# Optimization experiments

Measured on AMD Instinct MI355X. Metric: run time of the kernel, lower is better.

Reference implementation:

```python
import jax, jax.numpy as jnp
import numpy as np
from functools import partial

EDGES = [(1,2),(1,3),(1,4),(1,5),(1,6),(2,3),(2,7),(2,8),(3,4),(3,9),(4,5),(4,10),(5,6),(5,11),(6,12),(6,13),(7,8),(7,14),(8,9),(8,14),(9,10),(9,15),(10,11),(10,16),(11,12),(11,17),(12,13),(12,18),(13,18),(14,15),(14,19),(15,16),(15,19),(16,17),(16,20),(17,18),(17,21),(18,21),(19,20),(19,22),(20,21),(20,22),(21,22),(24,25),(24,29),(25,26),(25,29),(26,17),(26,30),(27,28),(27,31),(28,31),(29,30),(29,32),(30,31),(30,32),(31,32),(34,35),(34,39),(35,36),(35,39),(36,37),(36,30),(37,18),(37,41),(38,41),(39,40),(39,42),(30,41),(30,42),(31,42),(44,45),(44,49),(45,46),(45,49),(46,47),(46,50),(47,48),(47,51),(48,51),(49,50),(49,52),(50,51),(50,52),(51,52),(54,55),(54,59),(55,56),(55,59),(56,57),(56,60),(57,58),(57,61),(58,61),(59,60),(59,62),(50,61),(60,62),(61,62)]

B, C, T = 32, 64, 4000
F1, D, F2, NCLS = 8, 2, 16, 4
KLEN, GK = 64, 8


def _bn_pack(k, c):
    kg, kb = jax.random.split(k)
    g = jax.random.uniform(kg, (c,), minval=0.5, maxval=1.5)
    b = 0.1 * jax.random.normal(kb, (c,))
    return jnp.stack([g, b, jnp.zeros(c), jnp.ones(c)])  # gamma, beta, mean, var


def setup_inputs() -> dict:
    key = jax.random.key(0)
    ks = jax.random.split(key, 16)
    A = np.zeros((C, C), np.float32)
    for i, j in EDGES:
        A[i - 1, j - 1] = 1.0
        A[j - 1, i - 1] = 1.0
    np.fill_diagonal(A, 1.0)
    feat = F2 * ((T // 4 + 1) // 8)  # 16 * 125 = 2000
    s = 0.1
    return {
        "x": jax.random.normal(ks[0], (B, C, T), jnp.float32),
        "adjacency": jnp.asarray(A),
        "conv1_w": s * jax.random.normal(ks[1], (F1, 1, 1, KLEN), jnp.float32),
        "bnF1": jnp.stack([_bn_pack(jax.random.fold_in(ks[2], i), F1) for i in range(4)]),
        "imp": jax.random.normal(ks[3], (3, F1, C, C), jnp.float32),
        "gconv_w": s * jax.random.normal(ks[4], (3, F1, F1, 1, GK), jnp.float32),
        "dw_w": s * jax.random.normal(ks[5], (F1 * D, 1, C, 1), jnp.float32),
        "bn_sp": _bn_pack(ks[6], F1 * D),
        "sep_dw_w": s * jax.random.normal(ks[7], (F1 * D, 1, 1, 16), jnp.float32),
        "sep_pw_w": s * jax.random.normal(ks[8], (F2, F1 * D, 1, 1), jnp.float32),
        "bn_sep": _bn_pack(ks[9], F2),
        "fc_w": s * jax.random.normal(ks[10], (NCLS, feat), jnp.float32),
        "fc_b": jnp.zeros((NCLS,), jnp.float32),
    }


def _conv(x, w, pad, groups=1):
    return jax.lax.conv_general_dilated(
        x, w, (1, 1), pad, dimension_numbers=("NCHW", "OIHW", "NCHW"),
        feature_group_count=groups)


def _bn(x, p, eps=1e-3):
    g, b, m, v = p
    scale = g * jax.lax.rsqrt(v + eps)
    return x * scale[None, :, None, None] + (b - m * scale)[None, :, None, None]


def reference(x, adjacency, conv1_w, bnF1, imp, gconv_w, dw_w, bn_sp,
              sep_dw_w, sep_pw_w, bn_sep, fc_w, fc_b):
    Bv = x.shape[0]
    h = x[:, None, :, :]                                    # (B,1,C,T)
    h = _conv(h, conv1_w, [(0, 0), (31, 32)])                # 'same' for k=64
    h = _bn(h, bnF1[0])
    for l in range(3):                                       # GraphTemporalConvolution x3
        A = adjacency[None] * imp[l]                         # (F1,C,C) masked importance
        h = jnp.einsum("fcd,bfdt->bfct", A, h)
        h = _conv(h, gconv_w[l], [(0, 0), (3, 4)])           # 'same' for k=8
        h = jax.nn.elu(_bn(h, bnF1[l + 1]))
    # spatial depthwise conv with max-norm constraint (renorm, no grad through scale)
    norms = jnp.sqrt(jnp.sum(dw_w ** 2, axis=(1, 2, 3), keepdims=True))
    scale = jax.lax.stop_gradient(jnp.minimum(1.0, 1.0 / jnp.maximum(norms, 1e-7)))
    h = _conv(h, dw_w * scale, [(0, 0), (0, 0)], groups=F1)  # (B,F1*D,1,T)
    h = jax.nn.elu(_bn(h, bn_sp))
    h = h.reshape(Bv, F1 * D, 1, T // 4, 4).mean(-1)         # AvgPool (1,4)
    # separable conv
    h = _conv(h, sep_dw_w, [(0, 0), (8, 8)], groups=F1 * D)  # width T/4 + 1
    h = _conv(h, sep_pw_w, [(0, 0), (0, 0)])
    h = jax.nn.elu(_bn(h, bn_sep))
    W = h.shape[-1]
    Wp = (W // 8) * 8
    h = h[..., :Wp].reshape(Bv, F2, 1, Wp // 8, 8).mean(-1)  # AvgPool (1,8)
    feat = h.reshape(Bv, -1)
    return feat @ fc_w.T + fc_b
```

## Files before the change

### kernel.cpp

```cpp
#include <hip/hip_runtime.h>


#define B_   32
#define C_   64
#define T_   4000
#define F1_  8
#define TP_  1000
#define W2_  1001
#define MAXDEG 16
#define ROW4 130
#define ROWD 520

typedef _Float16 h16x2 __attribute__((ext_vector_type(2)));
typedef _Float16 f16x8 __attribute__((ext_vector_type(8)));
typedef float    f32x4 __attribute__((ext_vector_type(4)));
typedef __fp16   cvt16x2 __attribute__((ext_vector_type(2)));

static __device__ __forceinline__ float bf2f(unsigned short h) {
  union { unsigned int u; float f; } v; v.u = ((unsigned int)h) << 16; return v.f;
}
static __device__ __forceinline__ unsigned short f2bf(float f) {
  union { float f; unsigned int u; } v; v.f = f;
  unsigned int r = v.u + 0x7FFFu + ((v.u >> 16) & 1u);
  return (unsigned short)(r >> 16);
}
static __device__ __forceinline__ float lo_h(unsigned int u) {
  union { unsigned int u; _Float16 h[2]; } v; v.u = u; return (float)v.h[0];
}
static __device__ __forceinline__ unsigned int pack2h(float a, float b) {
  union { _Float16 h[2]; unsigned int u; } v;
  v.h[0] = (_Float16)a; v.h[1] = (_Float16)b; return v.u;
}
#if defined(__has_builtin) && __has_builtin(__builtin_amdgcn_cvt_pkrtz)
static __device__ __forceinline__ unsigned int pkh(float a, float b) {
  union { cvt16x2 h; unsigned int u; } v;
  v.h = __builtin_amdgcn_cvt_pkrtz(a, b);
  return v.u;
}
#else
static __device__ __forceinline__ unsigned int pkh(float a, float b) {
  return pack2h(a, b);
}
#endif
static __device__ __forceinline__ h16x2 as_h2(unsigned int u) {
  union { unsigned int u; h16x2 h; } v; v.u = u; return v.h;
}
static __device__ __forceinline__ unsigned int alignb(unsigned int hi,
                                                      unsigned int lo,
                                                      unsigned int s) {
  return (unsigned int)(((((unsigned long long)hi) << 32) | lo) >> s);
}
static __device__ __forceinline__ float swz8(float v) {
  union { float f; int i; } a; a.f = v;
  a.i = __builtin_amdgcn_ds_swizzle(a.i, 0x201F);
  return a.f;
}
#define PERM_LO(y, x) __builtin_amdgcn_perm((y), (x), 0x05040100u)
#define PERM_HI(y, x) __builtin_amdgcn_perm((y), (x), 0x07060302u)
#if defined(__has_builtin) && __has_builtin(__builtin_amdgcn_fdot2)
#define DOT2(a, b, c) __builtin_amdgcn_fdot2((a), (b), (c), false)
#else
static __device__ __forceinline__ float dot2_fb(h16x2 a, h16x2 b, float c) {
  return fmaf((float)a[0], (float)b[0], fmaf((float)a[1], (float)b[1], c));
}
#define DOT2(a, b, c) dot2_fb((a), (b), (c))
#endif
static __device__ __forceinline__ float eluf(float z) {
  return z > 0.0f ? z : __expf(z) - 1.0f;
}
static __device__ __forceinline__ float ldin(const void* p, int i, int isf32) {
  return isf32 ? ((const float*)p)[i] : bf2f(((const unsigned short*)p)[i]);
}

__global__ __launch_bounds__(256) void k0_setup(
    const void* __restrict__ adj, const void* __restrict__ imp,
    const void* __restrict__ dww, const void* __restrict__ w1,
    const void* __restrict__ bnF, const void* __restrict__ gw,
    const void* __restrict__ bnsp, const void* __restrict__ sdw,
    const void* __restrict__ pw, const void* __restrict__ bnsep,
    const void* __restrict__ fcw, const void* __restrict__ fcb,
    int* __restrict__ flag, int* __restrict__ deg, int* __restrict__ col,
    uint4* __restrict__ w1mf,
    uint4* __restrict__ wmf, float* __restrict__ dwn,
    float* __restrict__ sdwc, float* __restrict__ pwc,
    float* __restrict__ fcwc, float* __restrict__ fcbc,
    float* __restrict__ bnFs, float* __restrict__ bnsps,
    float* __restrict__ bnseps,
    unsigned int* __restrict__ dwph)
{
  __shared__ float dwr[1024];
  __shared__ float dsc[16];
  int tid = threadIdx.x;
  int isf32 = (((const float*)adj)[0] == 1.0f) ? 1 : 0;
  if (tid == 0) *flag = isf32;

  for (int idx = tid; idx < 128; idx += 256) {
    int kk = idx >> 6, l = idx & 63;
    int o = l & 15, q = l >> 4;
    uint4 v; v.x = 0u; v.y = 0u; v.z = 0u; v.w = 0u;
    if (o < 8) {
      int bi = o*64 + 32*kk + 8*q;
      v.x = pack2h(ldin(w1, bi+0, isf32), ldin(w1, bi+1, isf32));
      v.y = pack2h(ldin(w1, bi+2, isf32), ldin(w1, bi+3, isf32));
      v.z = pack2h(ldin(w1, bi+4, isf32), ldin(w1, bi+5, isf32));
      v.w = pack2h(ldin(w1, bi+6, isf32), ldin(w1, bi+7, isf32));
    }
    w1mf[idx] = v;
  }
  for (int idx = tid; idx < 384; idx += 256) {
    int lf = idx >> 6;
    int layer = lf >> 1, frag = lf & 1;
    int lane2 = idx & 63;
    int o = lane2 & 15, ii = (lane2 >> 4) + 4*frag;
    uint4 v; v.x = 0u; v.y = 0u; v.z = 0u; v.w = 0u;
    if (o < 8) {
      int bi = layer*512 + (o*8 + ii)*8;
      v.x = pack2h(ldin(gw, bi+0, isf32), ldin(gw, bi+1, isf32));
      v.y = pack2h(ldin(gw, bi+2, isf32), ldin(gw, bi+3, isf32));
      v.z = pack2h(ldin(gw, bi+4, isf32), ldin(gw, bi+5, isf32));
      v.w = pack2h(ldin(gw, bi+6, isf32), ldin(gw, bi+7, isf32));
    }
    wmf[idx] = v;
  }
  for (int i = tid; i < 256;  i += 256) sdwc[i] = ldin(sdw, i, isf32);
  for (int i = tid; i < 256;  i += 256) pwc[i]  = ldin(pw, i, isf32);
  for (int i = tid; i < 8000; i += 256) fcwc[i] = ldin(fcw, i, isf32);
  if (tid < 4) fcbc[tid] = ldin(fcb, tid, isf32);
  for (int i = tid; i < 1024; i += 256) dwr[i] = ldin(dww, i, isf32);

  if (tid < 64) {
    int c = tid, n = 0;
    for (int e = 0; e < MAXDEG; ++e) col[c*MAXDEG + e] = c;
    for (int d = 0; d < 64; ++d) {
      if (ldin(adj, c*64 + d, isf32) != 0.0f) {
        if (n < MAXDEG) col[c*MAXDEG + n] = d;
        ++n;
      }
    }
    deg[c] = n < MAXDEG ? n : MAXDEG;
  }
  __syncthreads();
  if (tid < 16) {
    float s2 = 0.0f;
    for (int c2 = 0; c2 < 64; ++c2) { float wv = dwr[tid*64 + c2]; s2 += wv*wv; }
    dsc[tid] = fminf(1.0f, 1.0f / fmaxf(sqrtf(s2), 1e-7f));
  }
  if (tid >= 64 && tid < 96) {
    int i = tid - 64, s = i >> 3, f = i & 7;
    float g = ldin(bnF, s*32 + f,      isf32);
    float b = ldin(bnF, s*32 + 8 + f,  isf32);
    float m = ldin(bnF, s*32 + 16 + f, isf32);
    float v = ldin(bnF, s*32 + 24 + f, isf32);
    float sc = g * rsqrtf(v + 1e-3f);
    bnFs[s*16 + f] = sc; bnFs[s*16 + 8 + f] = b - m*sc;
  }
  if (tid >= 96 && tid < 112) {
    int ch = tid - 96;
    float g = ldin(bnsp, ch, isf32), b = ldin(bnsp, 16 + ch, isf32);
    float m = ldin(bnsp, 32 + ch, isf32), v = ldin(bnsp, 48 + ch, isf32);
    float sc = g * rsqrtf(v + 1e-3f);
    bnsps[ch] = sc; bnsps[16 + ch] = b - m*sc;
  }
  if (tid >= 112 && tid < 128) {
    int ch = tid - 112;
    float g = ldin(bnsep, ch, isf32), b = ldin(bnsep, 16 + ch, isf32);
    float m = ldin(bnsep, 32 + ch, isf32), v = ldin(bnsep, 48 + ch, isf32);
    float sc = g * rsqrtf(v + 1e-3f);
    bnseps[ch] = sc; bnseps[16 + ch] = b - m*sc;
  }
  __syncthreads();
  for (int i = tid; i < 1024; i += 256) dwn[i] = dwr[i] * dsc[i >> 6];
  __syncthreads();
  for (int idx = tid; idx < 512; idx += 256) {
    int ch = idx >> 5, p = idx & 31;
    dwph[idx] = pack2h(dwr[ch*64 + 2*p]   * dsc[ch],
                       dwr[ch*64 + 2*p+1] * dsc[ch]);
  }
}

__global__ __launch_bounds__(256) void k0b_avals(
    const void* __restrict__ adj, const void* __restrict__ imp,
    const int* __restrict__ flag,
    const int* __restrict__ deg, const int* __restrict__ col,
    float* __restrict__ avals, unsigned int* __restrict__ avph)
{
  int combo = blockIdx.x * 256 + threadIdx.x;
  int isf32 = *flag;
  int c = combo & 63;
  int lf = combo >> 6;
  int dg = deg[c];
  float av[MAXDEG];
  for (int e = 0; e < MAXDEG; ++e) {
    float v = 0.0f;
    if (e < dg) {
      int d = col[c*MAXDEG + e];
      v = ldin(adj, c*64 + d, isf32) * ldin(imp, (lf*64 + c)*64 + d, isf32);
    }
    av[e] = v;
    avals[combo*MAXDEG + e] = v;
  }
  for (int p = 0; p < 8; ++p)
    avph[combo*8 + p] = pack2h(av[2*p], av[2*p + 1]);
}

__global__ __launch_bounds__(256, 4) void k1_conv1_bn(
    const void* __restrict__ x,
    const uint4* __restrict__ w1mf,
    const float* __restrict__ bnFs,
    const int* __restrict__ flag,
    unsigned short* __restrict__ outp)
{
  __shared__ __align__(16) unsigned int xs[548];
  int tid = threadIdx.x;
  int bc = blockIdx.y;
  int b = bc >> 6, c = bc & 63;
  int tb = blockIdx.x * 1024;
  int isf32 = *flag;
  int row = bc * T_;
  if (isf32) {
    const float* xr = (const float*)x + row;
    for (int m = tid; m < 274; m += 256) {
      int tg = tb - 36 + 4*m;
      uint2 st;
      if (tg >= 0 && tg + 3 < T_) {
        float4 v = *(const float4*)(xr + tg);
        st.x = pkh(v.x, v.y); st.y = pkh(v.z, v.w);
      } else {
        float q0 = (tg   >= 0 && tg   < T_) ? xr[tg]   : 0.0f;
        float q1 = (tg+1 >= 0 && tg+1 < T_) ? xr[tg+1] : 0.0f;
        float q2 = (tg+2 >= 0 && tg+2 < T_) ? xr[tg+2] : 0.0f;
        float q3 = (tg+3 >= 0 && tg+3 < T_) ? xr[tg+3] : 0.0f;
        st.x = pkh(q0, q1); st.y = pkh(q2, q3);
      }
      *(uint2*)(xs + 2*m) = st;
    }
  } else {
    const unsigned short* xr = (const unsigned short*)x + row;
    for (int m = tid; m < 274; m += 256) {
      int tg = tb - 36 + 4*m;
      uint2 st;
      if (tg >= 0 && tg + 3 < T_) {
        uint2 v = *(const uint2*)(xr + tg);
        st.x = pkh(bf2f((unsigned short)(v.x & 0xFFFFu)),
                   bf2f((unsigned short)(v.x >> 16)));
        st.y = pkh(bf2f((unsigned short)(v.y & 0xFFFFu)),
                   bf2f((unsigned short)(v.y >> 16)));
      } else {
        float q0 = (tg   >= 0 && tg   < T_) ? bf2f(xr[tg])   : 0.0f;
        float q1 = (tg+1 >= 0 && tg+1 < T_) ? bf2f(xr[tg+1]) : 0.0f;
        float q2 = (tg+2 >= 0 && tg+2 < T_) ? bf2f(xr[tg+2]) : 0.0f;
        float q3 = (tg+3 >= 0 && tg+3 < T_) ? bf2f(xr[tg+3]) : 0.0f;
        st.x = pkh(q0, q1); st.y = pkh(q2, q3);
      }
      *(uint2*)(xs + 2*m) = st;
    }
  }
  __syncthreads();

  int lane = tid & 63;
  int wv4 = tid >> 6;
  int m = lane & 15, q = lane >> 4;
  int sel = (m >> 3) & 1;
  union { uint4 u; f16x8 h; } w0u, w1u;
  w0u.u = w1mf[lane];
  w1u.u = w1mf[64 + lane];
  int o8 = m & 7;
  float sc  = bnFs[o8];
  float shb = bnFs[8 + o8];
  const unsigned int* p0 = xs + 2 + m + 4*q + 128*wv4;
  unsigned short* orow = outp + (size_t)((b*8 + o8)*64 + c) * T_;
  #pragma unroll
  for (int s = 0; s < 8; ++s) {
    unsigned dwa[5], dwb[5];
    #pragma unroll
    for (int j = 0; j < 5; ++j) {
      dwa[j] = p0[16*s + j];
      dwb[j] = p0[16*s + 16 + j];
    }
    union { unsigned d[4]; f16x8 h; } Ae0, Ao0, Ae1, Ao1;
    #pragma unroll
    for (int j = 0; j < 4; ++j) {
      Ao0.d[j] = dwa[j+1];
      Ae0.d[j] = alignb(dwa[j+1], dwa[j], 16);
      Ao1.d[j] = dwb[j+1];
      Ae1.d[j] = alignb(dwb[j+1], dwb[j], 16);
    }
    f32x4 ae = {0.0f, 0.0f, 0.0f, 0.0f};
    f32x4 ao = {0.0f, 0.0f, 0.0f, 0.0f};
    ae = __builtin_amdgcn_mfma_f32_16x16x32_f16(Ae0.h, w0u.h, ae, 0, 0, 0);
    ae = __builtin_amdgcn_mfma_f32_16x16x32_f16(Ae1.h, w1u.h, ae, 0, 0, 0);
    ao = __builtin_amdgcn_mfma_f32_16x16x32_f16(Ao0.h, w0u.h, ao, 0, 0, 0);
    ao = __builtin_amdgcn_mfma_f32_16x16x32_f16(Ao1.h, w1u.h, ao, 0, 0, 0);
    float r0 = swz8(ae[2]);
    float r1 = swz8(ao[2]);
    float r2 = swz8(ae[3]);
    float r3 = swz8(ao[3]);
    float y0 = sel ? r0 : ae[0];
    float y1 = sel ? r1 : ao[0];
    float y2 = sel ? r2 : ae[1];
    float y3 = sel ? r3 : ao[1];
    int t0g = tb + wv4*256 + s*32 + 8*q + 4*sel;
    if (t0g < T_) {
      uint2 st;
      st.x = pkh(y0*sc + shb, y1*sc + shb);
      st.y = pkh(y2*sc + shb, y3*sc + shb);
      *(uint2*)(orow + t0g) = st;
    }
  }
}

__global__ __launch_bounds__(256, 6) void k23_gcn_gconv(
    const unsigned short* __restrict__ in,
    unsigned short* __restrict__ outp,
    const int* __restrict__ deg, const int* __restrict__ col,
    const float* __restrict__ avals,
    const unsigned int* __restrict__ avph,
    const uint4* __restrict__ wmf,
    const float* __restrict__ bnFs, int l)
{
  __shared__ __align__(16) uint4 ash[8 * ROW4];
  int tid = threadIdx.x;
  int wgid = blockIdx.y * 4 + blockIdx.x;
  int swz  = (wgid & 7) * 1024 + (wgid >> 3);
  int c = swz & 63;
  int xt = (swz >> 6) & 3;
  int b = swz >> 8;
  int tb = xt * 1024;
  int wb = tb - 8;
  int dg = deg[c];
  const int* cp = col + c*MAXDEG;

  {
    int i = tid >> 5;
    int mlane = tid & 31;
    int dgp = (dg + 1) >> 1;
    const unsigned int* wpp = avph + ((l*8 + i)*64 + c) * 8;
    const float* av = avals + ((l*8 + i)*64 + c) * MAXDEG;
    const unsigned short* rbp = in + (size_t)((b*8 + i) * 64) * T_;
    for (int m = mlane; m < ROW4; m += 32) {
      int t = wb + 8*m;
      float a[8] = {0,0,0,0,0,0,0,0};
      if (t >= 0 && t + 7 < T_) {
        for (int p = 0; p < dgp; ++p) {
          int d0 = cp[2*p];
          int d1 = cp[2*p + 1];
          h16x2 w2 = as_h2(wpp[p]);
          uint4 v0 = *(const uint4*)(rbp + d0*T_ + t);
          uint4 v1 = *(const uint4*)(rbp + d1*T_ + t);
          a[0] = DOT2(as_h2(PERM_LO(v1.x, v0.x)), w2, a[0]);
          a[1] = DOT2(as_h2(PERM_HI(v1.x, v0.x)), w2, a[1]);
          a[2] = DOT2(as_h2(PERM_LO(v1.y, v0.y)), w2, a[2]);
          a[3] = DOT2(as_h2(PERM_HI(v1.y, v0.y)), w2, a[3]);
          a[4] = DOT2(as_h2(PERM_LO(v1.z, v0.z)), w2, a[4]);
          a[5] = DOT2(as_h2(PERM_HI(v1.z, v0.z)), w2, a[5]);
          a[6] = DOT2(as_h2(PERM_LO(v1.w, v0.w)), w2, a[6]);
          a[7] = DOT2(as_h2(PERM_HI(v1.w, v0.w)), w2, a[7]);
        }
      } else if (t + 7 >= 0 && t < T_) {
        for (int e = 0; e < dg; ++e) {
          int d = cp[e];
          float wv = av[e];
          const unsigned short* rp = rbp + d*T_;
          #pragma unroll
          for (int q = 0; q < 8; ++q) {
            int tq = t + q;
            if (tq >= 0 && tq < T_)
              a[q] = fmaf(wv, lo_h((unsigned int)rp[tq]), a[q]);
          }
        }
      }
      uint4 o;
      o.x = pkh(a[0], a[1]); o.y = pkh(a[2], a[3]);
      o.z = pkh(a[4], a[5]); o.w = pkh(a[6], a[7]);
      ash[i*ROW4 + m] = o;
    }
  }
  __syncthreads();

  int lane = tid & 63;
  int wv4 = tid >> 6;
  int m = lane & 15, q = lane >> 4;
  int sel = (m >> 3) & 1;
  union { uint4 u; f16x8 h; } w0u, w1u;
  w0u.u = wmf[(l*2 + 0)*64 + lane];
  w1u.u = wmf[(l*2 + 1)*64 + lane];
  int o8 = m & 7;
  float sc  = bnFs[(l+1)*16 + o8];
  float shb = bnFs[(l+1)*16 + 8 + o8];
  const unsigned int* ashd = (const unsigned int*)ash;
  const unsigned int* p0 = ashd + q*ROWD + wv4*128 + m + 2;
  const unsigned int* p1 = p0 + 4*ROWD;
  unsigned short* orow = outp + (size_t)((b*8 + o8)*64 + c) * T_;
  #pragma unroll
  for (int s = 0; s < 8; ++s) {
    unsigned dwa[5], dwb[5];
    #pragma unroll
    for (int j = 0; j < 5; ++j) {
      dwa[j] = p0[16*s + j];
      dwb[j] = p1[16*s + j];
    }
    union { unsigned d[4]; f16x8 h; } Ae0, Ao0, Ae1, Ao1;
    #pragma unroll
    for (int j = 0; j < 4; ++j) {
      Ao0.d[j] = dwa[j+1];
      Ae0.d[j] = alignb(dwa[j+1], dwa[j], 16);
      Ao1.d[j] = dwb[j+1];
      Ae1.d[j] = alignb(dwb[j+1], dwb[j], 16);
    }
    f32x4 ae = {0.0f, 0.0f, 0.0f, 0.0f};
    f32x4 ao = {0.0f, 0.0f, 0.0f, 0.0f};
    ae = __builtin_amdgcn_mfma_f32_16x16x32_f16(Ae0.h, w0u.h, ae, 0, 0, 0);
    ae = __builtin_amdgcn_mfma_f32_16x16x32_f16(Ae1.h, w1u.h, ae, 0, 0, 0);
    ao = __builtin_amdgcn_mfma_f32_16x16x32_f16(Ao0.h, w0u.h, ao, 0, 0, 0);
    ao = __builtin_amdgcn_mfma_f32_16x16x32_f16(Ao1.h, w1u.h, ao, 0, 0, 0);
    float r0 = swz8(ae[2]);
    float r1 = swz8(ao[2]);
    float r2 = swz8(ae[3]);
    float r3 = swz8(ao[3]);
    float y0 = sel ? r0 : ae[0];
    float y1 = sel ? r1 : ao[0];
    float y2 = sel ? r2 : ae[1];
    float y3 = sel ? r3 : ao[1];
    int t0g = tb + wv4*256 + s*32 + 8*q + 4*sel;
    if (t0g < T_) {
      uint2 st;
      st.x = pkh(eluf(y0*sc + shb), eluf(y1*sc + shb));
      st.y = pkh(eluf(y2*sc + shb), eluf(y3*sc + shb));
      *(uint2*)(orow + t0g) = st;
    }
  }
}

__global__ __launch_bounds__(256) void k4_dw(
    const unsigned short* __restrict__ in,
    const unsigned int* __restrict__ dwph,
    const float* __restrict__ bnsps,
    float* __restrict__ p1)
{
  int tid = threadIdx.x;
  int bg = blockIdx.y;
  int b = bg >> 3, g = bg & 7;
  int tile = blockIdx.x * 256 + tid;
  if (tile >= 500) return;
  int t0 = tile * 8;
  int base = bg * (64 * T_);
  const unsigned int* w0pp = dwph + (2*g)*32;
  const unsigned int* w1pp = dwph + (2*g + 1)*32;
  float a0[8] = {0,0,0,0,0,0,0,0}, a1[8] = {0,0,0,0,0,0,0,0};
  for (int p = 0; p < 32; ++p) {
    h16x2 w02 = as_h2(w0pp[p]);
    h16x2 w12 = as_h2(w1pp[p]);
    uint4 v0 = *(const uint4*)(in + base + (2*p)*T_ + t0);
    uint4 v1 = *(const uint4*)(in + base + (2*p + 1)*T_ + t0);
    unsigned pr;
    pr = PERM_LO(v1.x, v0.x);
    a0[0] = DOT2(as_h2(pr), w02, a0[0]); a1[0] = DOT2(as_h2(pr), w12, a1[0]);
    pr = PERM_HI(v1.x, v0.x);
    a0[1] = DOT2(as_h2(pr), w02, a0[1]); a1[1] = DOT2(as_h2(pr), w12, a1[1]);
    pr = PERM_LO(v1.y, v0.y);
    a0[2] = DOT2(as_h2(pr), w02, a0[2]); a1[2] = DOT2(as_h2(pr), w12, a1[2]);
    pr = PERM_HI(v1.y, v0.y);
    a0[3] = DOT2(as_h2(pr), w02, a0[3]); a1[3] = DOT2(as_h2(pr), w12, a1[3]);
    pr = PERM_LO(v1.z, v0.z);
    a0[4] = DOT2(as_h2(pr), w02, a0[4]); a1[4] = DOT2(as_h2(pr), w12, a1[4]);
    pr = PERM_HI(v1.z, v0.z);
    a0[5] = DOT2(as_h2(pr), w02, a0[5]); a1[5] = DOT2(as_h2(pr), w12, a1[5]);
    pr = PERM_LO(v1.w, v0.w);
    a0[6] = DOT2(as_h2(pr), w02, a0[6]); a1[6] = DOT2(as_h2(pr), w12, a1[6]);
    pr = PERM_HI(v1.w, v0.w);
    a0[7] = DOT2(as_h2(pr), w02, a0[7]); a1[7] = DOT2(as_h2(pr), w12, a1[7]);
  }
  float sc0 = bnsps[2*g],     sh0 = bnsps[16 + 2*g];
  float sc1 = bnsps[2*g + 1], sh1 = bnsps[16 + 2*g + 1];
  int oi = t0 >> 2;
  float2 r0, r1;
  r0.x = 0.25f * (eluf(a0[0]*sc0+sh0) + eluf(a0[1]*sc0+sh0)
                + eluf(a0[2]*sc0+sh0) + eluf(a0[3]*sc0+sh0));
  r0.y = 0.25f * (eluf(a0[4]*sc0+sh0) + eluf(a0[5]*sc0+sh0)
                + eluf(a0[6]*sc0+sh0) + eluf(a0[7]*sc0+sh0));
  r1.x = 0.25f * (eluf(a1[0]*sc1+sh1) + eluf(a1[1]*sc1+sh1)
                + eluf(a1[2]*sc1+sh1) + eluf(a1[3]*sc1+sh1));
  r1.y = 0.25f * (eluf(a1[4]*sc1+sh1) + eluf(a1[5]*sc1+sh1)
                + eluf(a1[6]*sc1+sh1) + eluf(a1[7]*sc1+sh1));
  *(float2*)(p1 + (b*16 + 2*g)*TP_ + oi)     = r0;
  *(float2*)(p1 + (b*16 + 2*g + 1)*TP_ + oi) = r1;
}

__global__ __launch_bounds__(256) void k5_sep(
    const float* __restrict__ p1,
    const float* __restrict__ sdwc,
    const float* __restrict__ pwc,
    const float* __restrict__ bnseps,
    float* __restrict__ p2)
{
  __shared__ float ps[16*272];
  int tid = threadIdx.x;
  int wq = blockIdx.x, b = blockIdx.y;
  int wb = wq * 256;
  for (int ch = 0; ch < 16; ++ch) {
    for (int s = tid; s < 272; s += 256) {
      int t = wb - 8 + s;
      ps[ch*272 + s] = (t >= 0 && t < TP_) ? p1[(b*16 + ch)*TP_ + t] : 0.0f;
    }
  }
  __syncthreads();
  int w0 = wb + tid;
  if (w0 >= W2_) return;
  float dws[16];
  for (int ch = 0; ch < 16; ++ch) {
    float a = 0.0f;
    #pragma unroll
    for (int k = 0; k < 16; ++k)
      a = fmaf(sdwc[ch*16 + k], ps[ch*272 + tid + k], a);
    dws[ch] = a;
  }
  for (int f = 0; f < 16; ++f) {
    float a = 0.0f;
    #pragma unroll
    for (int ch = 0; ch < 16; ++ch) a = fmaf(pwc[f*16 + ch], dws[ch], a);
    float sc = bnseps[f], sh = bnseps[16 + f];
    p2[(b*16 + f)*W2_ + w0] = eluf(a*sc + sh);
  }
}

__global__ __launch_bounds__(256) void k6_fc(
    const float* __restrict__ p2,
    const float* __restrict__ fcwc,
    const float* __restrict__ fcbc,
    const int* __restrict__ flag,
    void* __restrict__ outp)
{
  __shared__ float red[4*256];
  int tid = threadIdx.x;
  int b = blockIdx.x;
  float part[4] = {0.0f, 0.0f, 0.0f, 0.0f};
  for (int idx = tid; idx < 2000; idx += 256) {
    int f = idx / 125, q = idx - f*125;
    const float* src = p2 + (b*16 + f)*W2_ + q*8;
    float s = src[0]+src[1]+src[2]+src[3]+src[4]+src[5]+src[6]+src[7];
    float mval = 0.125f * s;
    #pragma unroll
    for (int n = 0; n < 4; ++n) part[n] = fmaf(fcwc[n*2000 + idx], mval, part[n]);
  }
  #pragma unroll
  for (int n = 0; n < 4; ++n) red[n*256 + tid] = part[n];
  __syncthreads();
  for (int s = 128; s > 0; s >>= 1) {
    if (tid < s) {
      #pragma unroll
      for (int n = 0; n < 4; ++n) red[n*256 + tid] += red[n*256 + tid + s];
    }
    __syncthreads();
  }
  if (tid < 4) {
    float val = red[tid*256] + fcbc[tid];
    if (*flag) ((float*)outp)[b*4 + tid] = val;
    else       ((unsigned short*)outp)[b*4 + tid] = f2bf(val);
  }
}

extern "C" void kernel_launch(void* const* d_in, const int* in_sizes, int n_in,
                              void* d_out, int out_size, void* d_ws, size_t ws_size,
                              hipStream_t stream) {
  const void* x     = d_in[0];
  const void* adj   = d_in[1];
  const void* w1    = d_in[2];
  const void* bnF   = d_in[3];
  const void* imp   = d_in[4];
  const void* gw    = d_in[5];
  const void* dww   = d_in[6];
  const void* bnsp  = d_in[7];
  const void* sdw   = d_in[8];
  const void* pw    = d_in[9];
  const void* bnsep = d_in[10];
  const void* fcw   = d_in[11];
  const void* fcb   = d_in[12];

  char* w = (char*)d_ws;
  const size_t OFF = 262144000;
  unsigned short* bufA = (unsigned short*)(w);
  unsigned short* bufB = (unsigned short*)(w + 131072000);
  int*   flag   = (int*)  (w + OFF + 0);
  int*   deg    = (int*)  (w + OFF + 256);
  int*   col    = (int*)  (w + OFF + 512);
  float* avals  = (float*)(w + OFF + 4608);
  float* dwn    = (float*)(w + OFF + 108032);
  float* sdwc   = (float*)(w + OFF + 112128);
  float* pwc    = (float*)(w + OFF + 113152);
  float* fcwc   = (float*)(w + OFF + 114176);
  float* fcbc   = (float*)(w + OFF + 146176);
  float* bnFs   = (float*)(w + OFF + 146432);
  float* bnsps  = (float*)(w + OFF + 146688);
  float* bnseps = (float*)(w + OFF + 146944);
  float* p1     = (float*)(w + OFF + 147200);
  float* p2     = (float*)(w + OFF + 2195200);
  uint4* wmf    = (uint4*)(w + OFF + 4245248);
  unsigned int* avph = (unsigned int*)(w + OFF + 4251392);
  unsigned int* dwph = (unsigned int*)(w + OFF + 4300544);
  uint4* w1mf   = (uint4*)(w + OFF + 4302592);

  k0_setup<<<1, 256, 0, stream>>>(adj, imp, dww, w1, bnF, gw, bnsp, sdw, pw,
                                  bnsep, fcw, fcb, flag, deg, col,
                                  w1mf, wmf, dwn, sdwc, pwc, fcwc, fcbc,
                                  bnFs, bnsps, bnseps, dwph);
  k0b_avals<<<6, 256, 0, stream>>>(adj, imp, flag, deg, col, avals, avph);
  k1_conv1_bn<<<dim3(4, B_*C_), 256, 0, stream>>>(x, w1mf, bnFs, flag, bufA);
  for (int l = 0; l < 3; ++l) {
    const unsigned short* src = (l & 1) ? bufB : bufA;
    unsigned short*       dst = (l & 1) ? bufA : bufB;
    k23_gcn_gconv<<<dim3(4, B_*C_), 256, 0, stream>>>(src, dst, deg, col,
                                                      avals, avph, wmf, bnFs, l);
  }
  k4_dw<<<dim3(2, B_*F1_), 256, 0, stream>>>(bufB, dwph, bnsps, p1);
  k5_sep<<<dim3(4, B_), 256, 0, stream>>>(p1, sdwc, pwc, bnseps, p2);
  k6_fc<<<32, 256, 0, stream>>>(p2, fcwc, fcbc, flag, d_out);
}
```

Baseline: 454.2 us.

## Replicate MFMA weight rows to drop swizzles, raise gconv occupancy, split k4 tiles

```diff
diff --git a/kernel.cpp b/kernel.cpp
--- a/kernel.cpp
+++ b/kernel.cpp
@@ -49,11 +49,6 @@
                                                       unsigned int lo,
                                                       unsigned int s) {
   return (unsigned int)(((((unsigned long long)hi) << 32) | lo) >> s);
-}
-static __device__ __forceinline__ float swz8(float v) {
-  union { float f; int i; } a; a.f = v;
-  a.i = __builtin_amdgcn_ds_swizzle(a.i, 0x201F);
-  return a.f;
 }
 #define PERM_LO(y, x) __builtin_amdgcn_perm((y), (x), 0x05040100u)
 #define PERM_HI(y, x) __builtin_amdgcn_perm((y), (x), 0x07060302u)
@@ -96,30 +91,26 @@
 
   for (int idx = tid; idx < 128; idx += 256) {
     int kk = idx >> 6, l = idx & 63;
-    int o = l & 15, q = l >> 4;
-    uint4 v; v.x = 0u; v.y = 0u; v.z = 0u; v.w = 0u;
-    if (o < 8) {
-      int bi = o*64 + 32*kk + 8*q;
-      v.x = pack2h(ldin(w1, bi+0, isf32), ldin(w1, bi+1, isf32));
-      v.y = pack2h(ldin(w1, bi+2, isf32), ldin(w1, bi+3, isf32));
-      v.z = pack2h(ldin(w1, bi+4, isf32), ldin(w1, bi+5, isf32));
-      v.w = pack2h(ldin(w1, bi+6, isf32), ldin(w1, bi+7, isf32));
-    }
+    int o = l & 7, q = (l >> 4) & 3;
+    uint4 v;
+    int bi = o*64 + 32*kk + 8*q;
+    v.x = pack2h(ldin(w1, bi+0, isf32), ldin(w1, bi+1, isf32));
+    v.y = pack2h(ldin(w1, bi+2, isf32), ldin(w1, bi+3, isf32));
+    v.z = pack2h(ldin(w1, bi+4, isf32), ldin(w1, bi+5, isf32));
+    v.w = pack2h(ldin(w1, bi+6, isf32), ldin(w1, bi+7, isf32));
     w1mf[idx] = v;
   }
   for (int idx = tid; idx < 384; idx += 256) {
     int lf = idx >> 6;
     int layer = lf >> 1, frag = lf & 1;
     int lane2 = idx & 63;
-    int o = lane2 & 15, ii = (lane2 >> 4) + 4*frag;
-    uint4 v; v.x = 0u; v.y = 0u; v.z = 0u; v.w = 0u;
-    if (o < 8) {
-      int bi = layer*512 + (o*8 + ii)*8;
-      v.x = pack2h(ldin(gw, bi+0, isf32), ldin(gw, bi+1, isf32));
-      v.y = pack2h(ldin(gw, bi+2, isf32), ldin(gw, bi+3, isf32));
-      v.z = pack2h(ldin(gw, bi+4, isf32), ldin(gw, bi+5, isf32));
-      v.w = pack2h(ldin(gw, bi+6, isf32), ldin(gw, bi+7, isf32));
-    }
+    int o = lane2 & 7, ii = (lane2 >> 4) + 4*frag;
+    uint4 v;
+    int bi = layer*512 + (o*8 + ii)*8;
+    v.x = pack2h(ldin(gw, bi+0, isf32), ldin(gw, bi+1, isf32));
+    v.y = pack2h(ldin(gw, bi+2, isf32), ldin(gw, bi+3, isf32));
+    v.z = pack2h(ldin(gw, bi+4, isf32), ldin(gw, bi+5, isf32));
+    v.w = pack2h(ldin(gw, bi+6, isf32), ldin(gw, bi+7, isf32));
     wmf[idx] = v;
   }
   for (int i = tid; i < 256;  i += 256) sdwc[i] = ldin(sdw, i, isf32);
@@ -291,14 +282,10 @@
     ae = __builtin_amdgcn_mfma_f32_16x16x32_f16(Ae1.h, w1u.h, ae, 0, 0, 0);
     ao = __builtin_amdgcn_mfma_f32_16x16x32_f16(Ao0.h, w0u.h, ao, 0, 0, 0);
     ao = __builtin_amdgcn_mfma_f32_16x16x32_f16(Ao1.h, w1u.h, ao, 0, 0, 0);
-    float r0 = swz8(ae[2]);
-    float r1 = swz8(ao[2]);
-    float r2 = swz8(ae[3]);
-    float r3 = swz8(ao[3]);
-    float y0 = sel ? r0 : ae[0];
-    float y1 = sel ? r1 : ao[0];
-    float y2 = sel ? r2 : ae[1];
-    float y3 = sel ? r3 : ao[1];
+    float y0 = sel ? ae[2] : ae[0];
+    float y1 = sel ? ao[2] : ao[0];
+    float y2 = sel ? ae[3] : ae[1];
+    float y3 = sel ? ao[3] : ao[1];
     int t0g = tb + wv4*256 + s*32 + 8*q + 4*sel;
     if (t0g < T_) {
       uint2 st;
@@ -309,7 +296,7 @@
   }
 }
 
-__global__ __launch_bounds__(256, 6) void k23_gcn_gconv(
+__global__ __launch_bounds__(256, 8) void k23_gcn_gconv(
     const unsigned short* __restrict__ in,
     unsigned short* __restrict__ outp,
     const int* __restrict__ deg, const int* __restrict__ col,
@@ -413,14 +400,10 @@
     ae = __builtin_amdgcn_mfma_f32_16x16x32_f16(Ae1.h, w1u.h, ae, 0, 0, 0);
     ao = __builtin_amdgcn_mfma_f32_16x16x32_f16(Ao0.h, w0u.h, ao, 0, 0, 0);
     ao = __builtin_amdgcn_mfma_f32_16x16x32_f16(Ao1.h, w1u.h, ao, 0, 0, 0);
-    float r0 = swz8(ae[2]);
-    float r1 = swz8(ao[2]);
-    float r2 = swz8(ae[3]);
-    float r3 = swz8(ao[3]);
-    float y0 = sel ? r0 : ae[0];
-    float y1 = sel ? r1 : ao[0];
-    float y2 = sel ? r2 : ae[1];
-    float y3 = sel ? r3 : ao[1];
+    float y0 = sel ? ae[2] : ae[0];
+    float y1 = sel ? ao[2] : ao[0];
+    float y2 = sel ? ae[3] : ae[1];
+    float y3 = sel ? ao[3] : ao[1];
     int t0g = tb + wv4*256 + s*32 + 8*q + 4*sel;
     if (t0g < T_) {
       uint2 st;
@@ -441,17 +424,17 @@
   int bg = blockIdx.y;
   int b = bg >> 3, g = bg & 7;
   int tile = blockIdx.x * 256 + tid;
-  if (tile >= 500) return;
-  int t0 = tile * 8;
+  if (tile >= 1000) return;
+  int t0 = tile * 4;
   int base = bg * (64 * T_);
   const unsigned int* w0pp = dwph + (2*g)*32;
   const unsigned int* w1pp = dwph + (2*g + 1)*32;
-  float a0[8] = {0,0,0,0,0,0,0,0}, a1[8] = {0,0,0,0,0,0,0,0};
+  float a0[4] = {0,0,0,0}, a1[4] = {0,0,0,0};
   for (int p = 0; p < 32; ++p) {
     h16x2 w02 = as_h2(w0pp[p]);
     h16x2 w12 = as_h2(w1pp[p]);
-    uint4 v0 = *(const uint4*)(in + base + (2*p)*T_ + t0);
-    uint4 v1 = *(const uint4*)(in + base + (2*p + 1)*T_ + t0);
+    uint2 v0 = *(const uint2*)(in + base + (2*p)*T_ + t0);
+    uint2 v1 = *(const uint2*)(in + base + (2*p + 1)*T_ + t0);
     unsigned pr;
     pr = PERM_LO(v1.x, v0.x);
     a0[0] = DOT2(as_h2(pr), w02, a0[0]); a1[0] = DOT2(as_h2(pr), w12, a1[0]);
@@ -461,29 +444,15 @@
     a0[2] = DOT2(as_h2(pr), w02, a0[2]); a1[2] = DOT2(as_h2(pr), w12, a1[2]);
     pr = PERM_HI(v1.y, v0.y);
     a0[3] = DOT2(as_h2(pr), w02, a0[3]); a1[3] = DOT2(as_h2(pr), w12, a1[3]);
-    pr = PERM_LO(v1.z, v0.z);
-    a0[4] = DOT2(as_h2(pr), w02, a0[4]); a1[4] = DOT2(as_h2(pr), w12, a1[4]);
-    pr = PERM_HI(v1.z, v0.z);
-    a0[5] = DOT2(as_h2(pr), w02, a0[5]); a1[5] = DOT2(as_h2(pr), w12, a1[5]);
-    pr = PERM_LO(v1.w, v0.w);
-    a0[6] = DOT2(as_h2(pr), w02, a0[6]); a1[6] = DOT2(as_h2(pr), w12, a1[6]);
-    pr = PERM_HI(v1.w, v0.w);
-    a0[7] = DOT2(as_h2(pr), w02, a0[7]); a1[7] = DOT2(as_h2(pr), w12, a1[7]);
   }
   float sc0 = bnsps[2*g],     sh0 = bnsps[16 + 2*g];
   float sc1 = bnsps[2*g + 1], sh1 = bnsps[16 + 2*g + 1];
-  int oi = t0 >> 2;
-  float2 r0, r1;
-  r0.x = 0.25f * (eluf(a0[0]*sc0+sh0) + eluf(a0[1]*sc0+sh0)
-                + eluf(a0[2]*sc0+sh0) + eluf(a0[3]*sc0+sh0));
-  r0.y = 0.25f * (eluf(a0[4]*sc0+sh0) + eluf(a0[5]*sc0+sh0)
-                + eluf(a0[6]*sc0+sh0) + eluf(a0[7]*sc0+sh0));
-  r1.x = 0.25f * (eluf(a1[0]*sc1+sh1) + eluf(a1[1]*sc1+sh1)
-                + eluf(a1[2]*sc1+sh1) + eluf(a1[3]*sc1+sh1));
-  r1.y = 0.25f * (eluf(a1[4]*sc1+sh1) + eluf(a1[5]*sc1+sh1)
-                + eluf(a1[6]*sc1+sh1) + eluf(a1[7]*sc1+sh1));
-  *(float2*)(p1 + (b*16 + 2*g)*TP_ + oi)     = r0;
-  *(float2*)(p1 + (b*16 + 2*g + 1)*TP_ + oi) = r1;
+  float r0 = 0.25f * (eluf(a0[0]*sc0+sh0) + eluf(a0[1]*sc0+sh0)
+                    + eluf(a0[2]*sc0+sh0) + eluf(a0[3]*sc0+sh0));
+  float r1 = 0.25f * (eluf(a1[0]*sc1+sh1) + eluf(a1[1]*sc1+sh1)
+                    + eluf(a1[2]*sc1+sh1) + eluf(a1[3]*sc1+sh1));
+  p1[(b*16 + 2*g)*TP_ + tile]     = r0;
+  p1[(b*16 + 2*g + 1)*TP_ + tile] = r1;
 }
 
 __global__ __launch_bounds__(256) void k5_sep(
@@ -611,7 +580,7 @@
     k23_gcn_gconv<<<dim3(4, B_*C_), 256, 0, stream>>>(src, dst, deg, col,
                                                       avals, avph, wmf, bnFs, l);
   }
-  k4_dw<<<dim3(2, B_*F1_), 256, 0, stream>>>(bufB, dwph, bnsps, p1);
+  k4_dw<<<dim3(4, B_*F1_), 256, 0, stream>>>(bufB, dwph, bnsps, p1);
   k5_sep<<<dim3(4, B_), 256, 0, stream>>>(p1, sdwc, pwc, bnseps, p2);
   k6_fc<<<32, 256, 0, stream>>>(p2, fcwc, fcbc, flag, d_out);
 }
```

After: 457.3 us. Within noise of the previous version (+0.7%).
